# Performance work log

Hardware: AMD Instinct MI355X
Metric: run time of the kernel (lower is better)

## Reference

```python
import jax, jax.numpy as jnp
import numpy as np

B, N, E = 4, 2048, 16384
D, DM, NH, DH, FE = 10, 256, 8, 32, 9
K, KHOP, SIGMA = 30, 3, 1.5
_HOP_W = np.exp(-(np.arange(1, KHOP + 1) ** 2) / (2.0 * SIGMA ** 2))
_HOP_Z = float(_HOP_W.sum())


def _ln(x, g, b):
    mu = x.mean(-1, keepdims=True)
    var = ((x - mu) ** 2).mean(-1, keepdims=True)
    return g * (x - mu) * jax.lax.rsqrt(var + 1e-5) + b


def setup_inputs() -> dict:
    key = jax.random.key(0)
    ks = jax.random.split(key, 40)
    s = 0.02
    inp = {
        'bus_type': jax.random.randint(ks[0], (B, N), 0, 4, dtype=jnp.int32),
        'edge_index': jax.random.randint(ks[1], (B, 2, E), 0, N, dtype=jnp.int32),
        'G': 0.05 * jax.random.normal(ks[2], (B, N, N), jnp.float32),
        'Bm': 0.05 * jax.random.normal(ks[3], (B, N, N), jnp.float32),
        'P_set': jax.random.normal(ks[4], (B, N), jnp.float32),
        'Q_set': jax.random.normal(ks[5], (B, N), jnp.float32),
        'V0': jnp.stack([0.9 + 0.2 * jax.random.uniform(ks[6], (B, N)),
                         0.2 * jax.random.uniform(ks[7], (B, N)) - 0.1], -1).astype(jnp.float32),
        'edge_feat': jax.random.normal(ks[8], (B, E, FE), jnp.float32),
        'Win': s * jax.random.normal(ks[9], (2 * (4 + D), DM), jnp.float32),
        'b_in': jnp.zeros((DM,), jnp.float32),
        'Wq': s * jax.random.normal(ks[10], (DM, DM), jnp.float32),
        'bq': jnp.zeros((DM,), jnp.float32),
        'Wk': s * jax.random.normal(ks[11], (DM, DM), jnp.float32),
        'bk': jnp.zeros((DM,), jnp.float32),
        'Wv': s * jax.random.normal(ks[12], (DM, DM), jnp.float32),
        'bv': jnp.zeros((DM,), jnp.float32),
        'Wo': s * jax.random.normal(ks[13], (DM, DM), jnp.float32),
        'bo': jnp.zeros((DM,), jnp.float32),
        'We': s * jax.random.normal(ks[14], (FE, NH), jnp.float32),
        'be': jnp.zeros((NH,), jnp.float32),
        'ln1_g': jnp.ones((DM,), jnp.float32),
        'ln1_b': jnp.zeros((DM,), jnp.float32),
        'ln2_g': jnp.ones((DM,), jnp.float32),
        'ln2_b': jnp.zeros((DM,), jnp.float32),
        'Wf1': s * jax.random.normal(ks[15], (DM, 4 * DM), jnp.float32),
        'bf1': jnp.zeros((4 * DM,), jnp.float32),
        'Wf2': s * jax.random.normal(ks[16], (4 * DM, DM), jnp.float32),
        'bf2': jnp.zeros((DM,), jnp.float32),
        'Wth': s * jax.random.normal(ks[17], (K, DM, 1), jnp.float32),
        'bth': jnp.zeros((K, 1), jnp.float32),
        'Wvh': s * jax.random.normal(ks[18], (K, DM, 1), jnp.float32),
        'bvh': jnp.zeros((K, 1), jnp.float32),
        'Wm': s * jax.random.normal(ks[19], (K, DM, D), jnp.float32),
        'bm': jnp.zeros((K, D), jnp.float32),
    }
    return inp


def reference(bus_type, edge_index, G, Bm, P_set, Q_set, V0, edge_feat,
              Win, b_in, Wq, bq, Wk, bk, Wv, bv, Wo, bo, We, be,
              ln1_g, ln1_b, ln2_g, ln2_b, Wf1, bf1, Wf2, bf2,
              Wth, bth, Wvh, bvh, Wm, bm):
    slack = bus_type == 1
    pv = bus_type == 2
    p_maskf = (~slack).astype(G.dtype)            # theta updates / DP mask
    q_maskf = (~(slack | pv)).astype(G.dtype)     # v updates / DQ mask

    # electrical transition matrix T = rownorm(|Y| with zero diag), khop_source='yabs', khop_norm='row'
    A = jnp.sqrt(G * G + Bm * Bm) * (1.0 - jnp.eye(N, dtype=G.dtype))
    T = A / jnp.clip(A.sum(-1, keepdims=True), 1e-12, None)

    # flattened directed edges across batch for segment ops
    src = edge_index[:, 0, :]
    dst = edge_index[:, 1, :]
    offs = (jnp.arange(B, dtype=src.dtype) * N)[:, None]
    src_f = (src + offs).reshape(-1)
    dst_f = (dst + offs).reshape(-1)
    eb_f = (edge_feat @ We + be).reshape(-1, NH)  # per-edge per-head attention bias

    def khop(X):  # Gaussian-weighted K-hop diffusion: sum_h w_h T^h X / sum_h w_h
        Hh, acc = X, jnp.zeros_like(X)
        for hop in range(KHOP):
            Hh = jnp.einsum('bij,bjf->bif', T, Hh)
            acc = acc + float(_HOP_W[hop]) * Hh
        return acc / _HOP_Z

    def attn_block(x):  # edge-sparse multi-head self-attention + FFN
        q = (x @ Wq + bq).reshape(B * N, NH, DH)
        k = (x @ Wk + bk).reshape(B * N, NH, DH)
        vv = (x @ Wv + bv).reshape(B * N, NH, DH)
        score = (q[dst_f] * k[src_f]).sum(-1) / np.sqrt(DH) + eb_f  # [B*E, NH]
        mx = jax.ops.segment_max(score, dst_f, num_segments=B * N)
        p = jnp.exp(score - mx[dst_f])
        den = jax.ops.segment_sum(p, dst_f, num_segments=B * N)
        alpha = p / den[dst_f]
        agg = jax.ops.segment_sum(alpha[:, :, None] * vv[src_f], dst_f, num_segments=B * N)
        x = _ln(x + agg.reshape(B, N, DM) @ Wo + bo, ln1_g, ln1_b)
        h = jax.nn.relu(x @ Wf1 + bf1)
        return _ln(x + h @ Wf2 + bf2, ln2_g, ln2_b)

    def step(carry, hp):
        v, th, m = carry
        Wth_k, bth_k, Wvh_k, bvh_k, Wm_k, bm_k = hp
        e = v * jnp.cos(th)
        f = v * jnp.sin(th)
        Ire = jnp.einsum('bij,bj->bi', G, e) - jnp.einsum('bij,bj->bi', Bm, f)
        Iim = jnp.einsum('bij,bj->bi', G, f) + jnp.einsum('bij,bj->bi', Bm, e)
        DP = (P_set - (e * Ire + f * Iim)) * p_maskf
        DQ = (Q_set - (f * Ire - e * Iim)) * q_maskf
        ns = jnp.concatenate([jnp.stack([v, th, DP, DQ], -1), m], -1)  # [B,N,4+D]
        x = jnp.concatenate([ns, khop(ns)], -1) @ Win + b_in
        x = attn_block(x)
        dth = (x @ Wth_k + bth_k)[..., 0]
        dv = (x @ Wvh_k + bvh_k)[..., 0]
        m_new = x @ Wm_k + bm_k
        return (v + dv * q_maskf, th + dth * p_maskf, m_new), None

    v0, th0 = V0[..., 0], V0[..., 1]
    m0 = jnp.zeros((B, N, D), dtype=V0.dtype)
    (v, th, _), _ = jax.lax.scan(step, (v0, th0, m0), (Wth, bth, Wvh, bvh, Wm, bm))
    return jnp.stack([v, th], -1)
```

## Files before the change

kernel.cpp:

```cpp
#include <hip/hip_runtime.h>
#include <math.h>

typedef _Float16 f16x8 __attribute__((ext_vector_type(8)));
typedef _Float16 f16x4 __attribute__((ext_vector_type(4)));
typedef float f32x4 __attribute__((ext_vector_type(4)));

constexpr int B_ = 4, N_ = 2048, E_ = 16384;
constexpr int D_ = 10, DM_ = 256, NH_ = 8, FE_ = 9;
constexpr int BN_ = B_ * N_;
constexpr int BE_ = B_ * E_;

#define DEVI __device__ __forceinline__

DEVI _Float16 f2h(float f) { return (_Float16)f; }


__global__ void init_state(const int* __restrict__ bus, const float* __restrict__ V0,
                           float* v, float* th, float* m, float* pm, float* qm,
                           int* counts) {
  int t = blockIdx.x * blockDim.x + threadIdx.x;
  if (t >= BN_) return;
  int bt = bus[t];
  pm[t] = (bt == 1) ? 0.f : 1.f;
  qm[t] = (bt == 1 || bt == 2) ? 0.f : 1.f;
  v[t] = V0[2 * t];
  th[t] = V0[2 * t + 1];
  for (int d = 0; d < D_; ++d) m[(size_t)t * D_ + d] = 0.f;
  counts[t] = 0;
}

__global__ __launch_bounds__(256) void build_T_cast(const float* __restrict__ G,
    const float* __restrict__ Bm, _Float16* __restrict__ Tb,
    _Float16* __restrict__ Gh, _Float16* __restrict__ Bh) {
  int row = blockIdx.x;
  int i = row & (N_ - 1);
  const float* Gr = G + (size_t)row * N_;
  const float* Br = Bm + (size_t)row * N_;
  float a[8];
  float s = 0.f;
#pragma unroll
  for (int u = 0; u < 8; ++u) {
    int j = threadIdx.x + u * 256;
    float g = Gr[j], b = Br[j];
    if (Gh) { Gh[(size_t)row * N_ + j] = f2h(g); Bh[(size_t)row * N_ + j] = f2h(b); }
    float av = sqrtf(g * g + b * b);
    if (j == i) av = 0.f;
    a[u] = av;
    s += av;
  }
  __shared__ float red[4];
  for (int off = 32; off; off >>= 1) s += __shfl_down(s, off);
  int lane = threadIdx.x & 63, wave = threadIdx.x >> 6;
  if (lane == 0) red[wave] = s;
  __syncthreads();
  float tot = red[0] + red[1] + red[2] + red[3];
  float inv = 1.f / fmaxf(tot, 1e-12f);
#pragma unroll
  for (int u = 0; u < 8; ++u) {
    int j = threadIdx.x + u * 256;
    Tb[(size_t)row * N_ + j] = f2h(a[u] * inv);
  }
}

__global__ __launch_bounds__(256) void transpose16(const _Float16* __restrict__ in,
                                                   _Float16* __restrict__ out) {
  __shared__ float tile[64][65];
  int b = blockIdx.z;
  const _Float16* A = in + (size_t)b * N_ * N_;
  _Float16* O = out + (size_t)b * N_ * N_;
  int r0 = blockIdx.y * 64, c0 = blockIdx.x * 64;
  int tc = threadIdx.x & 63, tg = threadIdx.x >> 6;
#pragma unroll
  for (int i = 0; i < 16; ++i) {
    int r = tg * 16 + i;
    tile[r][tc] = (float)A[(size_t)(r0 + r) * N_ + c0 + tc];
  }
  __syncthreads();
#pragma unroll
  for (int i = 0; i < 16; ++i) {
    int r = tg * 16 + i;
    O[(size_t)(c0 + r) * N_ + r0 + tc] = f2h(tile[tc][r]);
  }
}

__global__ __launch_bounds__(256) void gemm_bat(const _Float16* __restrict__ A,
    const _Float16* __restrict__ Bt, _Float16* __restrict__ Cout,
    const _Float16* __restrict__ M1, const _Float16* __restrict__ M2,
    float w1, float w2, float w3) {
  int b = blockIdx.z;
  const _Float16* Ab = A + (size_t)b * N_ * N_;
  const _Float16* Bb = Bt + (size_t)b * N_ * N_;
  int wave = threadIdx.x >> 6, lane = threadIdx.x & 63;
  int wy = wave >> 1, wx = wave & 1;
  int m0 = blockIdx.x * 64 + wy * 32;
  int n0 = blockIdx.y * 64 + wx * 32;
  int lm = lane & 15, lq = lane >> 4;
  f32x4 acc[2][2] = {};
  const _Float16* A0 = Ab + (size_t)(m0 + lm) * N_ + lq * 8;
  const _Float16* A1 = A0 + (size_t)16 * N_;
  const _Float16* B0 = Bb + (size_t)(n0 + lm) * N_ + lq * 8;
  const _Float16* B1 = B0 + (size_t)16 * N_;
  for (int k = 0; k < N_; k += 32) {
    f16x8 a0 = *(const f16x8*)(A0 + k);
    f16x8 a1 = *(const f16x8*)(A1 + k);
    f16x8 b0 = *(const f16x8*)(B0 + k);
    f16x8 b1 = *(const f16x8*)(B1 + k);
    acc[0][0] = __builtin_amdgcn_mfma_f32_16x16x32_f16(a0, b0, acc[0][0], 0, 0, 0);
    acc[0][1] = __builtin_amdgcn_mfma_f32_16x16x32_f16(a0, b1, acc[0][1], 0, 0, 0);
    acc[1][0] = __builtin_amdgcn_mfma_f32_16x16x32_f16(a1, b0, acc[1][0], 0, 0, 0);
    acc[1][1] = __builtin_amdgcn_mfma_f32_16x16x32_f16(a1, b1, acc[1][1], 0, 0, 0);
  }
  _Float16* Cb = Cout + (size_t)b * N_ * N_;
#pragma unroll
  for (int tm = 0; tm < 2; ++tm)
#pragma unroll
    for (int tn = 0; tn < 2; ++tn) {
      int col = n0 + tn * 16 + lm;
#pragma unroll
      for (int r = 0; r < 4; ++r) {
        int row = m0 + tm * 16 + lq * 4 + r;
        size_t o = (size_t)b * N_ * N_ + (size_t)row * N_ + col;
        float val = acc[tm][tn][r];
        if (M1) val = w3 * val + w1 * (float)M1[o] + w2 * (float)M2[o];
        Cb[(size_t)row * N_ + col] = f2h(val);
      }
    }
}

__global__ void edge_prep(const int* __restrict__ ei, const float* __restrict__ efeat,
    const float* __restrict__ We, const float* __restrict__ be,
    float* __restrict__ eb, int* __restrict__ srcf, int* __restrict__ dstf,
    int* __restrict__ counts) {
  int t = blockIdx.x * blockDim.x + threadIdx.x;
  if (t >= BE_) return;
  int b = t / E_, e = t - b * E_;
  int src = ei[(size_t)b * 2 * E_ + e];
  int dst = ei[(size_t)b * 2 * E_ + E_ + e];
  srcf[t] = src + b * N_;
  int df = dst + b * N_;
  dstf[t] = df;
  atomicAdd(&counts[df], 1);
  float fv[FE_];
#pragma unroll
  for (int f = 0; f < FE_; ++f) fv[f] = efeat[(size_t)t * FE_ + f];
#pragma unroll
  for (int h = 0; h < NH_; ++h) {
    float s = be[h];
#pragma unroll
    for (int f = 0; f < FE_; ++f) s += fv[f] * We[f * NH_ + h];
    eb[(size_t)t * NH_ + h] = s;
  }
}

__global__ void scan_kernel(const int* __restrict__ counts, int* __restrict__ offs,
                            int* __restrict__ cursor) {
  __shared__ int part[256];
  int t = threadIdx.x;
  int base = t * 32;
  int loc[32];
  int s = 0;
#pragma unroll
  for (int i = 0; i < 32; ++i) { loc[i] = counts[base + i]; s += loc[i]; }
  part[t] = s;
  __syncthreads();
  for (int off = 1; off < 256; off <<= 1) {
    int vv = (t >= off) ? part[t - off] : 0;
    __syncthreads();
    part[t] += vv;
    __syncthreads();
  }
  int run = part[t] - s;
#pragma unroll
  for (int i = 0; i < 32; ++i) {
    offs[base + i] = run;
    cursor[base + i] = run;
    run += loc[i];
  }
  if (t == 255) offs[BN_] = run;
}

__global__ void scatter_kernel(const int* __restrict__ dstf, int* cursor,
                               int* __restrict__ perm) {
  int t = blockIdx.x * blockDim.x + threadIdx.x;
  if (t >= BE_) return;
  int d = dstf[t];
  int pos = atomicAdd(&cursor[d], 1);
  perm[pos] = t;
}

__global__ void edge_reorder(const int* __restrict__ perm, const int* __restrict__ srcf,
                             const float* __restrict__ eb, int* __restrict__ sp,
                             float* __restrict__ ebp) {
  int j = blockIdx.x * 256 + threadIdx.x;
  if (j >= BE_) return;
  int e = perm[j];
  sp[j] = srcf[e];
#pragma unroll
  for (int h = 0; h < NH_; ++h) ebp[(size_t)j * 8 + h] = eb[(size_t)e * 8 + h];
}

__global__ void prep_weights(const float* Wq, const float* bq, const float* Wk,
    const float* bk, const float* Wv, const float* bvv, const float* Wo,
    const float* Wf1, const float* Wf2, const float* Wth, const float* bth,
    const float* Wvh, const float* bvh, const float* Wm, const float* bm,
    const float* Win,
    _Float16* Wqkvt, float* bqkv, _Float16* Wot,
    _Float16* Wf1t, _Float16* Wf2t, float* Wheads, float* bheads,
    _Float16* Wint) {
  int i = blockIdx.x * blockDim.x + threadIdx.x;
  if (i < 768 * 256) {
    int n = i >> 8, kk = i & 255;
    float val = n < 256 ? Wq[kk * 256 + n]
              : n < 512 ? Wk[kk * 256 + (n - 256)] : Wv[kk * 256 + (n - 512)];
    Wqkvt[n * 256 + kk] = f2h(val);
    return;
  }
  i -= 768 * 256;
  if (i < 256 * 256) {
    int n = i >> 8, kk = i & 255;
    Wot[n * 256 + kk] = f2h(Wo[kk * 256 + n]);
    return;
  }
  i -= 256 * 256;
  if (i < 1024 * 256) {
    int n = i >> 8, kk = i & 255;
    Wf1t[n * 256 + kk] = f2h(Wf1[kk * 1024 + n]);
    return;
  }
  i -= 1024 * 256;
  if (i < 256 * 1024) {
    int n = i >> 10, kk = i & 1023;
    Wf2t[n * 1024 + kk] = f2h(Wf2[kk * 256 + n]);
    return;
  }
  i -= 256 * 1024;
  if (i < 30 * 3072) {
    int k = i / 3072, j = i - k * 3072;
    int row = j / 12, o = j - row * 12;
    float val = o == 0 ? Wth[k * 256 + row]
              : o == 1 ? Wvh[k * 256 + row] : Wm[k * 2560 + row * 10 + (o - 2)];
    Wheads[k * 3072 + j] = val;
    return;
  }
  i -= 30 * 3072;
  if (i < 360) {
    int k = i / 12, o = i - k * 12;
    bheads[i] = o == 0 ? bth[k] : o == 1 ? bvh[k] : bm[k * 10 + (o - 2)];
    return;
  }
  i -= 360;
  if (i < 768) {
    bqkv[i] = i < 256 ? bq[i] : i < 512 ? bk[i - 256] : bvv[i - 512];
    return;
  }
  i -= 768;
  if (i < 256 * 32) {
    int n = i >> 5, kk = i & 31;
    Wint[n * 32 + kk] = (kk < 28) ? f2h(Win[kk * 256 + n]) : (_Float16)0.f;
  }
}


DEVI void ns_epilogue(int b, int row, float sre, float sim, int lane,
                      const float2* sef, const float* v, const float* th,
                      const float* P, const float* Q, const float* pm,
                      const float* qm, const float* m, _Float16* nsT) {
  for (int off = 1; off < 64; off <<= 1) {
    sre += __shfl_xor(sre, off);
    sim += __shfl_xor(sim, off);
  }
  if (lane < 16) {
    int node = b * N_ + row;
    float val;
    if (lane == 0) val = v[node];
    else if (lane == 1) val = th[node];
    else if (lane == 2) {
      float2 ef = sef[row];
      val = (P[node] - (ef.x * sre + ef.y * sim)) * pm[node];
    } else if (lane == 3) {
      float2 ef = sef[row];
      val = (Q[node] - (ef.y * sre - ef.x * sim)) * qm[node];
    } else if (lane < 14) val = m[(size_t)node * 10 + (lane - 4)];
    else val = 0.f;
    nsT[(size_t)b * 16 * N_ + (size_t)lane * N_ + row] = f2h(val);
  }
}

__global__ __launch_bounds__(256) void matvec_ns_f16(const _Float16* __restrict__ Gh,
    const _Float16* __restrict__ Bh, const float* __restrict__ v,
    const float* __restrict__ th, const float* __restrict__ P,
    const float* __restrict__ Q, const float* __restrict__ pm,
    const float* __restrict__ qm, const float* __restrict__ m,
    _Float16* __restrict__ nsT) {
  int b = blockIdx.y;
  __shared__ float2 sef[N_];
  for (int i = threadIdx.x; i < N_; i += 256) {
    float vv = v[b * N_ + i], tt = th[b * N_ + i];
    float sn, cs;
    __sincosf(tt, &sn, &cs);
    sef[i] = make_float2(vv * cs, vv * sn);
  }
  __syncthreads();
  int wave = threadIdx.x >> 6, lane = threadIdx.x & 63;
  for (int rr = 0; rr < 4; ++rr) {
    int row = blockIdx.x * 16 + wave * 4 + rr;
    const _Float16* Gr = Gh + ((size_t)b * N_ + row) * N_;
    const _Float16* Br = Bh + ((size_t)b * N_ + row) * N_;
    float sre = 0.f, sim = 0.f;
#pragma unroll
    for (int jj = 0; jj < 4; ++jj) {
      int j = lane * 8 + jj * 512;
      f16x8 g8 = *(const f16x8*)(Gr + j);
      f16x8 b8 = *(const f16x8*)(Br + j);
#pragma unroll
      for (int u = 0; u < 8; ++u) {
        float g = (float)g8[u], bb = (float)b8[u];
        float2 ef = sef[j + u];
        sre += g * ef.x - bb * ef.y;
        sim += g * ef.y + bb * ef.x;
      }
    }
    ns_epilogue(b, row, sre, sim, lane, sef, v, th, P, Q, pm, qm, m, nsT);
  }
}

__global__ __launch_bounds__(256) void matvec_ns_f32(const float* __restrict__ G,
    const float* __restrict__ Bm, const float* __restrict__ v,
    const float* __restrict__ th, const float* __restrict__ P,
    const float* __restrict__ Q, const float* __restrict__ pm,
    const float* __restrict__ qm, const float* __restrict__ m,
    _Float16* __restrict__ nsT) {
  int b = blockIdx.y;
  __shared__ float2 sef[N_];
  for (int i = threadIdx.x; i < N_; i += 256) {
    float vv = v[b * N_ + i], tt = th[b * N_ + i];
    float sn, cs;
    __sincosf(tt, &sn, &cs);
    sef[i] = make_float2(vv * cs, vv * sn);
  }
  __syncthreads();
  int wave = threadIdx.x >> 6, lane = threadIdx.x & 63;
  for (int rr = 0; rr < 4; ++rr) {
    int row = blockIdx.x * 16 + wave * 4 + rr;
    const float* Gr = G + ((size_t)b * N_ + row) * N_;
    const float* Br = Bm + ((size_t)b * N_ + row) * N_;
    float sre = 0.f, sim = 0.f;
#pragma unroll
    for (int jj = 0; jj < 8; ++jj) {
      int j = lane * 4 + jj * 256;
      float4 g4 = *(const float4*)(Gr + j);
      float4 b4 = *(const float4*)(Br + j);
      float2 e0 = sef[j], e1 = sef[j + 1], e2 = sef[j + 2], e3 = sef[j + 3];
      sre += g4.x * e0.x - b4.x * e0.y + g4.y * e1.x - b4.y * e1.y
           + g4.z * e2.x - b4.z * e2.y + g4.w * e3.x - b4.w * e3.y;
      sim += g4.x * e0.y + b4.x * e0.x + g4.y * e1.y + b4.y * e1.x
           + g4.z * e2.y + b4.z * e2.x + g4.w * e3.y + b4.w * e3.x;
    }
    ns_epilogue(b, row, sre, sim, lane, sef, v, th, P, Q, pm, qm, m, nsT);
  }
}

DEVI float khop_tile(const _Float16* __restrict__ Tm, const _Float16* __restrict__ Hin,
                     int b, int m0, int wave, int lm, int lq, int tid,
                     float (*red)[16][17]) {
  f32x4 acc = {0.f, 0.f, 0.f, 0.f};
  const _Float16* Trow = Tm + ((size_t)b * N_ + m0 + lm) * N_ + wave * 512 + lq * 8;
  const _Float16* Hrow = Hin + ((size_t)b * 16 + lm) * N_ + wave * 512 + lq * 8;
#pragma unroll 4
  for (int k = 0; k < 512; k += 32) {
    f16x8 a = *(const f16x8*)(Trow + k);
    f16x8 hb = *(const f16x8*)(Hrow + k);
    acc = __builtin_amdgcn_mfma_f32_16x16x32_f16(a, hb, acc, 0, 0, 0);
  }
#pragma unroll
  for (int r = 0; r < 4; ++r) red[wave][lq * 4 + r][lm] = acc[r];
  __syncthreads();
  int c = tid >> 4, rr = tid & 15;
  float s = red[0][rr][c] + red[1][rr][c] + red[2][rr][c] + red[3][rr][c];
  __syncthreads();
  return s;
}

__global__ __launch_bounds__(256) void khop_mix_input(
    const _Float16* __restrict__ Tmix, const _Float16* __restrict__ nsT,
    const _Float16* __restrict__ Wint, const float* __restrict__ bin,
    float* __restrict__ x0, _Float16* __restrict__ xh) {
  int b = blockIdx.y, m0 = blockIdx.x * 16;
  int tid = threadIdx.x;
  int wave = tid >> 6, lane = tid & 63;
  int lm = lane & 15, lq = lane >> 4;
  __shared__ float red[4][16][17];
  __shared__ _Float16 in28s[16][32];
  float s = khop_tile(Tmix, nsT, b, m0, wave, lm, lq, tid, red);
  int oc = tid >> 4, orr = tid & 15;
  size_t oidx = ((size_t)b * 16 + oc) * N_ + m0 + orr;
  if (oc < 14) {
    in28s[orr][oc] = nsT[oidx];
    in28s[orr][14 + oc] = f2h(s);
  } else if (oc == 14) {
    in28s[orr][28] = (_Float16)0.f;
    in28s[orr][29] = (_Float16)0.f;
  } else {
    in28s[orr][30] = (_Float16)0.f;
    in28s[orr][31] = (_Float16)0.f;
  }
  __syncthreads();
  f16x8 afrag = *(const f16x8*)(&in28s[lm][lq * 8]);
#pragma unroll
  for (int nt = 0; nt < 4; ++nt) {
    int n0 = wave * 64 + nt * 16;
    f16x8 bfrag = *(const f16x8*)(Wint + (size_t)(n0 + lm) * 32 + lq * 8);
    f32x4 c4 = {0.f, 0.f, 0.f, 0.f};
    c4 = __builtin_amdgcn_mfma_f32_16x16x32_f16(afrag, bfrag, c4, 0, 0, 0);
    float bv = bin[n0 + lm];
#pragma unroll
    for (int rg = 0; rg < 4; ++rg) {
      int rw = lq * 4 + rg;
      float val = c4[rg] + bv;
      size_t o = ((size_t)(b * N_ + m0 + rw)) * 256 + n0 + lm;
      x0[o] = val;
      xh[o] = f2h(val);
    }
  }
}

__global__ __launch_bounds__(256) void khop_kernel(const _Float16* __restrict__ Tb,
    const _Float16* __restrict__ HinT, _Float16* __restrict__ HoutT,
    float* __restrict__ accT, float w, int first) {
  int b = blockIdx.y, m0 = blockIdx.x * 16;
  int tid = threadIdx.x;
  int wave = tid >> 6, lane = tid & 63;
  int lm = lane & 15, lq = lane >> 4;
  __shared__ float red[4][16][17];
  float s = khop_tile(Tb, HinT, b, m0, wave, lm, lq, tid, red);
  int c = tid >> 4, r = tid & 15;
  size_t o = ((size_t)b * 16 + c) * N_ + m0 + r;
  if (HoutT) HoutT[o] = f2h(s);
  if (first) accT[o] = w * s; else accT[o] += w * s;
}

__global__ __launch_bounds__(256) void khop3_input(const _Float16* __restrict__ Tb,
    const _Float16* __restrict__ HinT, const _Float16* __restrict__ nsT,
    const float* __restrict__ accT, const _Float16* __restrict__ Wint,
    const float* __restrict__ bin, float hw2,
    float* __restrict__ x0, _Float16* __restrict__ xh) {
  int b = blockIdx.y, m0 = blockIdx.x * 16;
  int tid = threadIdx.x;
  int wave = tid >> 6, lane = tid & 63;
  int lm = lane & 15, lq = lane >> 4;
  __shared__ float red[4][16][17];
  __shared__ _Float16 in28s[16][32];
  float s = khop_tile(Tb, HinT, b, m0, wave, lm, lq, tid, red);
  int oc = tid >> 4, orr = tid & 15;
  size_t oidx = ((size_t)b * 16 + oc) * N_ + m0 + orr;
  if (oc < 14) {
    float atot = accT[oidx] + hw2 * s;
    in28s[orr][oc] = nsT[oidx];
    in28s[orr][14 + oc] = f2h(atot);
  } else if (oc == 14) {
    in28s[orr][28] = (_Float16)0.f;
    in28s[orr][29] = (_Float16)0.f;
  } else {
    in28s[orr][30] = (_Float16)0.f;
    in28s[orr][31] = (_Float16)0.f;
  }
  __syncthreads();
  f16x8 afrag = *(const f16x8*)(&in28s[lm][lq * 8]);
#pragma unroll
  for (int nt = 0; nt < 4; ++nt) {
    int n0 = wave * 64 + nt * 16;
    f16x8 bfrag = *(const f16x8*)(Wint + (size_t)(n0 + lm) * 32 + lq * 8);
    f32x4 c4 = {0.f, 0.f, 0.f, 0.f};
    c4 = __builtin_amdgcn_mfma_f32_16x16x32_f16(afrag, bfrag, c4, 0, 0, 0);
    float bv = bin[n0 + lm];
#pragma unroll
    for (int rg = 0; rg < 4; ++rg) {
      int rw = lq * 4 + rg;
      float val = c4[rg] + bv;
      size_t o = ((size_t)(b * N_ + m0 + rw)) * 256 + n0 + lm;
      x0[o] = val;
      xh[o] = f2h(val);
    }
  }
}

__global__ __launch_bounds__(256) void gemm_kernel(const _Float16* __restrict__ A,
    const _Float16* __restrict__ Wt, const float* __restrict__ bias,
    float* __restrict__ Cf, _Float16* __restrict__ Ch,
    int N, int K, int relu) {
  int wave = threadIdx.x >> 6, lane = threadIdx.x & 63;
  int wy = wave >> 1, wx = wave & 1;
  int m0 = blockIdx.x * 64 + wy * 32;
  int n0 = blockIdx.y * 64 + wx * 32;
  int lm = lane & 15, lq = lane >> 4;
  f32x4 acc[2][2] = {};
  const _Float16* A0 = A + (size_t)(m0 + lm) * K + lq * 8;
  const _Float16* A1 = A0 + (size_t)16 * K;
  const _Float16* B0 = Wt + (size_t)(n0 + lm) * K + lq * 8;
  const _Float16* B1 = B0 + (size_t)16 * K;
  for (int k = 0; k < K; k += 32) {
    f16x8 a0 = *(const f16x8*)(A0 + k);
    f16x8 a1 = *(const f16x8*)(A1 + k);
    f16x8 b0 = *(const f16x8*)(B0 + k);
    f16x8 b1 = *(const f16x8*)(B1 + k);
    acc[0][0] = __builtin_amdgcn_mfma_f32_16x16x32_f16(a0, b0, acc[0][0], 0, 0, 0);
    acc[0][1] = __builtin_amdgcn_mfma_f32_16x16x32_f16(a0, b1, acc[0][1], 0, 0, 0);
    acc[1][0] = __builtin_amdgcn_mfma_f32_16x16x32_f16(a1, b0, acc[1][0], 0, 0, 0);
    acc[1][1] = __builtin_amdgcn_mfma_f32_16x16x32_f16(a1, b1, acc[1][1], 0, 0, 0);
  }
#pragma unroll
  for (int tm = 0; tm < 2; ++tm)
#pragma unroll
    for (int tn = 0; tn < 2; ++tn) {
      int col = n0 + tn * 16 + lm;
      float bvv = bias ? bias[col] : 0.f;
#pragma unroll
      for (int r = 0; r < 4; ++r) {
        int row = m0 + tm * 16 + lq * 4 + r;
        float val = acc[tm][tn][r] + bvv;
        if (relu) val = fmaxf(val, 0.f);
        size_t o = (size_t)row * N + col;
        if (Cf) Cf[o] = val;
        if (Ch) Ch[o] = f2h(val);
      }
    }
}

__global__ __launch_bounds__(256) void attn_kernel(const _Float16* __restrict__ qkv,
    const int* __restrict__ offs, const int* __restrict__ sp,
    const float* __restrict__ ebp, _Float16* __restrict__ aggh) {
  int node = blockIdx.x * 4 + (threadIdx.x >> 6);
  int lane = threadIdx.x & 63;
  int h = lane >> 3;
  f16x4 qh = *(const f16x4*)(qkv + (size_t)node * 768 + lane * 4);
  float4 q4 = {(float)qh[0], (float)qh[1], (float)qh[2], (float)qh[3]};
  int beg = offs[node], end = offs[node + 1];
  float mx = -3.0e38f, den = 0.f;
  float4 acc = {0.f, 0.f, 0.f, 0.f};
  f16x4 kh_n = {}, vh_n = {};
  float eb_n = 0.f;
  if (beg < end) {
    int s = sp[beg];
    const _Float16* base = qkv + (size_t)s * 768 + lane * 4;
    kh_n = *(const f16x4*)(base + 256);
    vh_n = *(const f16x4*)(base + 512);
    eb_n = ebp[(size_t)beg * 8 + h];
  }
  for (int j = beg; j < end; ++j) {
    f16x4 kh = kh_n, vh = vh_n;
    float ebv = eb_n;
    if (j + 1 < end) {
      int s2 = sp[j + 1];
      const _Float16* b2 = qkv + (size_t)s2 * 768 + lane * 4;
      kh_n = *(const f16x4*)(b2 + 256);
      vh_n = *(const f16x4*)(b2 + 512);
      eb_n = ebp[(size_t)(j + 1) * 8 + h];
    }
    float p = q4.x * (float)kh[0] + q4.y * (float)kh[1]
            + q4.z * (float)kh[2] + q4.w * (float)kh[3];
    p += __shfl_xor(p, 1);
    p += __shfl_xor(p, 2);
    p += __shfl_xor(p, 4);
    float score = p * 0.17677669529663687f + ebv;
    float nm = fmaxf(mx, score);
    float sc = __expf(mx - nm);
    float w = __expf(score - nm);
    den = den * sc + w;
    acc.x = acc.x * sc + w * (float)vh[0];
    acc.y = acc.y * sc + w * (float)vh[1];
    acc.z = acc.z * sc + w * (float)vh[2];
    acc.w = acc.w * sc + w * (float)vh[3];
    mx = nm;
  }
  float inv = den > 0.f ? 1.f / den : 0.f;
  f16x4 o;
  o[0] = f2h(acc.x * inv);
  o[1] = f2h(acc.y * inv);
  o[2] = f2h(acc.z * inv);
  o[3] = f2h(acc.w * inv);
  *(f16x4*)(aggh + (size_t)node * DM_ + lane * 4) = o;
}

__global__ __launch_bounds__(256) void oproj_ln1(const _Float16* __restrict__ A,
    const _Float16* __restrict__ Wt, const float* __restrict__ bias,
    const float* __restrict__ res, const float* __restrict__ g,
    const float* __restrict__ bb, float* __restrict__ yF,
    _Float16* __restrict__ yH) {
  int m0 = blockIdx.x * 16;
  int wave = threadIdx.x >> 6, lane = threadIdx.x & 63;
  int lm = lane & 15, lq = lane >> 4;
  int n0 = wave * 64;
  f32x4 acc[4] = {};
  const _Float16* Ap = A + (size_t)(m0 + lm) * 256 + lq * 8;
  const _Float16* Bp = Wt + (size_t)(n0 + lm) * 256 + lq * 8;
  for (int k = 0; k < 256; k += 32) {
    f16x8 a0 = *(const f16x8*)(Ap + k);
#pragma unroll
    for (int nt = 0; nt < 4; ++nt) {
      f16x8 bf = *(const f16x8*)(Bp + nt * 16 * 256 + k);
      acc[nt] = __builtin_amdgcn_mfma_f32_16x16x32_f16(a0, bf, acc[nt], 0, 0, 0);
    }
  }
  float val[4][4];
  float rsum[4] = {}, rsq[4] = {};
#pragma unroll
  for (int nt = 0; nt < 4; ++nt) {
    int col = n0 + nt * 16 + lm;
    float bv = bias[col];
#pragma unroll
    for (int rg = 0; rg < 4; ++rg) {
      int row = m0 + lq * 4 + rg;
      float x = acc[nt][rg] + bv + res[(size_t)row * 256 + col];
      val[nt][rg] = x;
      rsum[rg] += x;
      rsq[rg] += x * x;
    }
  }
#pragma unroll
  for (int rg = 0; rg < 4; ++rg)
    for (int off = 1; off < 16; off <<= 1) {
      rsum[rg] += __shfl_xor(rsum[rg], off);
      rsq[rg] += __shfl_xor(rsq[rg], off);
    }
  __shared__ float redS[16][4], redQ[16][4];
  if (lm == 0) {
#pragma unroll
    for (int rg = 0; rg < 4; ++rg) {
      int r = lq * 4 + rg;
      redS[r][wave] = rsum[rg];
      redQ[r][wave] = rsq[rg];
    }
  }
  __syncthreads();
#pragma unroll
  for (int rg = 0; rg < 4; ++rg) {
    int r = lq * 4 + rg;
    float tS = redS[r][0] + redS[r][1] + redS[r][2] + redS[r][3];
    float tQ = redQ[r][0] + redQ[r][1] + redQ[r][2] + redQ[r][3];
    float mu = tS * (1.f / 256.f);
    float var = tQ * (1.f / 256.f) - mu * mu;
    float rs = rsqrtf(var + 1e-5f);
    int row = m0 + r;
#pragma unroll
    for (int nt = 0; nt < 4; ++nt) {
      int col = n0 + nt * 16 + lm;
      float y = g[col] * (val[nt][rg] - mu) * rs + bb[col];
      size_t o = (size_t)row * 256 + col;
      yF[o] = y;
      yH[o] = f2h(y);
    }
  }
}

__global__ __launch_bounds__(512) void ffn_fused(const _Float16* __restrict__ A,
    const _Float16* __restrict__ Wf1t, const float* __restrict__ bf1,
    const _Float16* __restrict__ Wf2t, const float* __restrict__ bf2,
    const float* __restrict__ res, const float* __restrict__ g,
    const float* __restrict__ bb, const float* __restrict__ Wh,
    const float* __restrict__ bh, const float* __restrict__ pm,
    const float* __restrict__ qm, float* __restrict__ v,
    float* __restrict__ th, float* __restrict__ m) {
  constexpr int HP = 1032;
  int m0 = blockIdx.x * 32;
  int tid = threadIdx.x;
  int wave = tid >> 6, lane = tid & 63;
  int lm = lane & 15, lq = lane >> 4;
  __shared__ _Float16 hs[32][HP];
  __shared__ float xs[32][261];
  __shared__ float whs[3072];
  __shared__ float part[32][193];
  __shared__ float redS[32][8], redQ[32][8];
  for (int i = tid; i < 3072; i += 512) whs[i] = Wh[i];
  {
    int n0 = wave * 128;
    f32x4 acc1[2][8] = {};
    const _Float16* Ap = A + (size_t)(m0 + lm) * 256 + lq * 8;
    const _Float16* Bp = Wf1t + (size_t)(n0 + lm) * 256 + lq * 8;
    for (int k = 0; k < 256; k += 32) {
      f16x8 a0 = *(const f16x8*)(Ap + k);
      f16x8 a1 = *(const f16x8*)(Ap + 16 * 256 + k);
#pragma unroll
      for (int nt = 0; nt < 8; ++nt) {
        f16x8 bf = *(const f16x8*)(Bp + nt * 16 * 256 + k);
        acc1[0][nt] = __builtin_amdgcn_mfma_f32_16x16x32_f16(a0, bf, acc1[0][nt], 0, 0, 0);
        acc1[1][nt] = __builtin_amdgcn_mfma_f32_16x16x32_f16(a1, bf, acc1[1][nt], 0, 0, 0);
      }
    }
#pragma unroll
    for (int mt = 0; mt < 2; ++mt)
#pragma unroll
      for (int nt = 0; nt < 8; ++nt) {
        int col = n0 + nt * 16 + lm;
        float bv = bf1[col];
#pragma unroll
        for (int rg = 0; rg < 4; ++rg) {
          int rloc = mt * 16 + lq * 4 + rg;
          hs[rloc][col] = f2h(fmaxf(acc1[mt][nt][rg] + bv, 0.f));
        }
      }
  }
  __syncthreads();
  float val[2][2][4];
  float rsum[2][4] = {}, rsq[2][4] = {};
  {
    int n0 = wave * 32;
    f32x4 acc2[2][2] = {};
    const _Float16* Bp = Wf2t + (size_t)(n0 + lm) * 1024 + lq * 8;
    for (int k = 0; k < 1024; k += 32) {
      f16x8 a0 = *(const f16x8*)(&hs[lm][k + lq * 8]);
      f16x8 a1 = *(const f16x8*)(&hs[16 + lm][k + lq * 8]);
      f16x8 b0 = *(const f16x8*)(Bp + k);
      f16x8 b1 = *(const f16x8*)(Bp + 16 * 1024 + k);
      acc2[0][0] = __builtin_amdgcn_mfma_f32_16x16x32_f16(a0, b0, acc2[0][0], 0, 0, 0);
      acc2[0][1] = __builtin_amdgcn_mfma_f32_16x16x32_f16(a0, b1, acc2[0][1], 0, 0, 0);
      acc2[1][0] = __builtin_amdgcn_mfma_f32_16x16x32_f16(a1, b0, acc2[1][0], 0, 0, 0);
      acc2[1][1] = __builtin_amdgcn_mfma_f32_16x16x32_f16(a1, b1, acc2[1][1], 0, 0, 0);
    }
#pragma unroll
    for (int mt = 0; mt < 2; ++mt)
#pragma unroll
      for (int nt = 0; nt < 2; ++nt) {
        int col = n0 + nt * 16 + lm;
        float bv = bf2[col];
#pragma unroll
        for (int rg = 0; rg < 4; ++rg) {
          int row = m0 + mt * 16 + lq * 4 + rg;
          float x = acc2[mt][nt][rg] + bv + res[(size_t)row * 256 + col];
          val[mt][nt][rg] = x;
          rsum[mt][rg] += x;
          rsq[mt][rg] += x * x;
        }
      }
  }
#pragma unroll
  for (int mt = 0; mt < 2; ++mt)
#pragma unroll
    for (int rg = 0; rg < 4; ++rg)
      for (int off = 1; off < 16; off <<= 1) {
        rsum[mt][rg] += __shfl_xor(rsum[mt][rg], off);
        rsq[mt][rg] += __shfl_xor(rsq[mt][rg], off);
      }
  if (lm == 0) {
#pragma unroll
    for (int mt = 0; mt < 2; ++mt)
#pragma unroll
      for (int rg = 0; rg < 4; ++rg) {
        int r = mt * 16 + lq * 4 + rg;
        redS[r][wave] = rsum[mt][rg];
        redQ[r][wave] = rsq[mt][rg];
      }
  }
  __syncthreads();
#pragma unroll
  for (int mt = 0; mt < 2; ++mt)
#pragma unroll
    for (int rg = 0; rg < 4; ++rg) {
      int r = mt * 16 + lq * 4 + rg;
      float tS = 0.f, tQ = 0.f;
#pragma unroll
      for (int w = 0; w < 8; ++w) { tS += redS[r][w]; tQ += redQ[r][w]; }
      float mu = tS * (1.f / 256.f);
      float var = tQ * (1.f / 256.f) - mu * mu;
      float rs = rsqrtf(var + 1e-5f);
#pragma unroll
      for (int nt = 0; nt < 2; ++nt) {
        int col = wave * 32 + nt * 16 + lm;
        xs[r][col] = g[col] * (val[mt][nt][rg] - mu) * rs + bb[col];
      }
    }
  __syncthreads();
  {
    int rw = tid & 31, grp = tid >> 5;
    float pa[12] = {};
    for (int c = 0; c < 16; ++c) {
      int col = grp * 16 + c;
      float xv = xs[rw][col];
#pragma unroll
      for (int o = 0; o < 12; ++o) pa[o] += xv * whs[col * 12 + o];
    }
#pragma unroll
    for (int o = 0; o < 12; ++o) part[rw][grp * 12 + o] = pa[o];
  }
  __syncthreads();
  if (tid < 32) {
    int node = m0 + tid;
    float tot[12];
#pragma unroll
    for (int o = 0; o < 12; ++o) {
      float s = bh[o];
#pragma unroll
      for (int grp = 0; grp < 16; ++grp) s += part[tid][grp * 12 + o];
      tot[o] = s;
    }
    th[node] += tot[0] * pm[node];
    v[node] += tot[1] * qm[node];
#pragma unroll
    for (int d = 0; d < 10; ++d) m[(size_t)node * 10 + d] = tot[2 + d];
  }
}

__global__ void out_kernel(const float* __restrict__ v, const float* __restrict__ th,
                           float* __restrict__ out) {
  int t = blockIdx.x * blockDim.x + threadIdx.x;
  if (t >= BN_) return;
  out[2 * t] = v[t];
  out[2 * t + 1] = th[t];
}


extern "C" void kernel_launch(void* const* d_in, const int* in_sizes, int n_in,
                              void* d_out, int out_size, void* d_ws, size_t ws_size,
                              hipStream_t stream) {
  const int* bus = (const int*)d_in[0];
  const int* ei = (const int*)d_in[1];
  const float* G = (const float*)d_in[2];
  const float* Bm = (const float*)d_in[3];
  const float* P = (const float*)d_in[4];
  const float* Q = (const float*)d_in[5];
  const float* V0 = (const float*)d_in[6];
  const float* efeat = (const float*)d_in[7];
  const float* Win = (const float*)d_in[8];
  const float* bin = (const float*)d_in[9];
  const float* Wq = (const float*)d_in[10];
  const float* bq = (const float*)d_in[11];
  const float* Wk = (const float*)d_in[12];
  const float* bk = (const float*)d_in[13];
  const float* Wv = (const float*)d_in[14];
  const float* bv = (const float*)d_in[15];
  const float* Wo = (const float*)d_in[16];
  const float* bo = (const float*)d_in[17];
  const float* We = (const float*)d_in[18];
  const float* be = (const float*)d_in[19];
  const float* g1 = (const float*)d_in[20];
  const float* b1 = (const float*)d_in[21];
  const float* g2 = (const float*)d_in[22];
  const float* b2 = (const float*)d_in[23];
  const float* Wf1 = (const float*)d_in[24];
  const float* bf1 = (const float*)d_in[25];
  const float* Wf2 = (const float*)d_in[26];
  const float* bf2 = (const float*)d_in[27];
  const float* Wth = (const float*)d_in[28];
  const float* bth = (const float*)d_in[29];
  const float* Wvh = (const float*)d_in[30];
  const float* bvh = (const float*)d_in[31];
  const float* Wm = (const float*)d_in[32];
  const float* bm = (const float*)d_in[33];
  float* out = (float*)d_out;

  char* p = (char*)d_ws;
  auto alloc = [&](size_t bytes) -> void* {
    void* r = (void*)p;
    p += (bytes + 255) & ~(size_t)255;
    return r;
  };
  _Float16* Tb = (_Float16*)alloc((size_t)BN_ * N_ * 2);
  _Float16* nsT = (_Float16*)alloc((size_t)B_ * 16 * N_ * 2);
  _Float16* H1 = (_Float16*)alloc((size_t)B_ * 16 * N_ * 2);
  _Float16* H2 = (_Float16*)alloc((size_t)B_ * 16 * N_ * 2);
  float* accT = (float*)alloc((size_t)B_ * 16 * N_ * 4);
  _Float16* qkvh = (_Float16*)alloc((size_t)BN_ * 768 * 2);
  float* x0 = (float*)alloc((size_t)BN_ * 256 * 4);
  float* x1 = (float*)alloc((size_t)BN_ * 256 * 4);
  _Float16* xhA = (_Float16*)alloc((size_t)BN_ * 256 * 2);
  _Float16* xhB = (_Float16*)alloc((size_t)BN_ * 256 * 2);
  float* eb = (float*)alloc((size_t)BE_ * 8 * 4);
  float* ebp = (float*)alloc((size_t)BE_ * 8 * 4);
  int* srcf = (int*)alloc((size_t)BE_ * 4);
  int* dstf = (int*)alloc((size_t)BE_ * 4);
  int* sp = (int*)alloc((size_t)BE_ * 4);
  int* counts = (int*)alloc((size_t)BN_ * 4);
  int* offs = (int*)alloc((size_t)(BN_ + 1) * 4);
  int* cursor = (int*)alloc((size_t)BN_ * 4);
  int* perm = (int*)alloc((size_t)BE_ * 4);
  _Float16* Wqkvt = (_Float16*)alloc(768 * 256 * 2);
  _Float16* Wot = (_Float16*)alloc(256 * 256 * 2);
  _Float16* Wf1t = (_Float16*)alloc(1024 * 256 * 2);
  _Float16* Wf2t = (_Float16*)alloc(256 * 1024 * 2);
  _Float16* Wint = (_Float16*)alloc(256 * 32 * 2);
  float* Wheads = (float*)alloc(30 * 3072 * 4);
  float* bheads = (float*)alloc(30 * 12 * 4);
  float* bqkv = (float*)alloc(768 * 4);
  float* v = (float*)alloc((size_t)BN_ * 4);
  float* th = (float*)alloc((size_t)BN_ * 4);
  float* pm = (float*)alloc((size_t)BN_ * 4);
  float* qm = (float*)alloc((size_t)BN_ * 4);
  float* m = (float*)alloc((size_t)BN_ * 10 * 4);

  size_t nn2 = (size_t)B_ * N_ * N_ * 2;
  size_t used = (size_t)(p - (char*)d_ws);
  bool tmix_ok = (used + 3 * (nn2 + 256) <= ws_size);
  _Float16 *Tt = nullptr, *T2 = nullptr, *Tmix = nullptr;
  if (tmix_ok) {
    Tt = (_Float16*)alloc(nn2);
    T2 = (_Float16*)alloc(nn2);
    Tmix = (_Float16*)alloc(nn2);
  }
  used = (size_t)(p - (char*)d_ws);
  bool f16gb = (used + 2 * (nn2 + 256) <= ws_size);
  _Float16 *Gh = nullptr, *Bh = nullptr;
  if (f16gb) {
    Gh = (_Float16*)alloc(nn2);
    Bh = (_Float16*)alloc(nn2);
  }

  double hwd[3], z = 0.0;
  for (int i = 0; i < 3; ++i) {
    hwd[i] = exp(-((double)(i + 1) * (i + 1)) / (2.0 * 1.5 * 1.5));
    z += hwd[i];
  }
  float hw0 = (float)(hwd[0] / z), hw1 = (float)(hwd[1] / z), hw2 = (float)(hwd[2] / z);

  init_state<<<32, 256, 0, stream>>>(bus, V0, v, th, m, pm, qm, counts);
  build_T_cast<<<8192, 256, 0, stream>>>(G, Bm, Tb, Gh, Bh);
  if (tmix_ok) {
    transpose16<<<dim3(32, 32, 4), 256, 0, stream>>>(Tb, Tt);
    gemm_bat<<<dim3(32, 32, 4), 256, 0, stream>>>(Tb, Tt, T2,
        (const _Float16*)nullptr, (const _Float16*)nullptr, 0.f, 0.f, 0.f);
    gemm_bat<<<dim3(32, 32, 4), 256, 0, stream>>>(T2, Tt, Tmix, Tb, T2,
                                                  hw0, hw1, hw2);
  }
  edge_prep<<<BE_ / 256, 256, 0, stream>>>(ei, efeat, We, be, eb, srcf, dstf, counts);
  scan_kernel<<<1, 256, 0, stream>>>(counts, offs, cursor);
  scatter_kernel<<<BE_ / 256, 256, 0, stream>>>(dstf, cursor, perm);
  edge_reorder<<<BE_ / 256, 256, 0, stream>>>(perm, srcf, eb, sp, ebp);
  prep_weights<<<(887912 + 255) / 256, 256, 0, stream>>>(
      Wq, bq, Wk, bk, Wv, bv, Wo, Wf1, Wf2, Wth, bth, Wvh, bvh, Wm, bm, Win,
      Wqkvt, bqkv, Wot, Wf1t, Wf2t, Wheads, bheads, Wint);

  for (int k = 0; k < 30; ++k) {
    if (f16gb)
      matvec_ns_f16<<<dim3(128, 4), 256, 0, stream>>>(Gh, Bh, v, th, P, Q, pm, qm,
                                                      m, nsT);
    else
      matvec_ns_f32<<<dim3(128, 4), 256, 0, stream>>>(G, Bm, v, th, P, Q, pm, qm,
                                                      m, nsT);
    if (tmix_ok) {
      khop_mix_input<<<dim3(128, 4), 256, 0, stream>>>(Tmix, nsT, Wint, bin,
                                                       x0, xhA);
    } else {
      khop_kernel<<<dim3(128, 4), 256, 0, stream>>>(Tb, nsT, H1, accT, hw0, 1);
      khop_kernel<<<dim3(128, 4), 256, 0, stream>>>(Tb, H1, H2, accT, hw1, 0);
      khop3_input<<<dim3(128, 4), 256, 0, stream>>>(Tb, H2, nsT, accT, Wint, bin,
                                                    hw2, x0, xhA);
    }
    gemm_kernel<<<dim3(128, 12), 256, 0, stream>>>(xhA, Wqkvt, bqkv, nullptr, qkvh,
                                                   768, 256, 0);
    attn_kernel<<<2048, 256, 0, stream>>>(qkvh, offs, sp, ebp, xhB);
    oproj_ln1<<<512, 256, 0, stream>>>(xhB, Wot, bo, x0, g1, b1, x1, xhA);
    ffn_fused<<<256, 512, 0, stream>>>(xhA, Wf1t, bf1, Wf2t, bf2, x1, g2, b2,
                                       Wheads + k * 3072, bheads + k * 12,
                                       pm, qm, v, th, m);
  }
  out_kernel<<<32, 256, 0, stream>>>(v, th, out);
}
```

Before: 4.791 ms.

## Enlarge batched GEMM tiles to 128x128 and overlay FFN shared buffers

The batched T·T GEMM used to precompute the k-hop mixing matrix now gives each wave a 64x64 output tile, 4x4 MFMA accumulators, instead of 32x32. The launch grid shrinks to match. This quarters the number of blocks and raises register-level reuse of each loaded A/B fragment, cutting redundant global loads. In the fused FFN kernel, the f16 hidden buffer and the later LayerNorm/head buffers now share one union in LDS, and the head-weight load moves after the second GEMM. This lowers shared-memory footprint, which could allow more blocks per CU. The costs are higher register pressure in the GEMM and fewer blocks to fill the GPU.

Result: faster. 4.618 ms (-3.6%).

```diff
diff --git a/kernel.cpp b/kernel.cpp
--- a/kernel.cpp
+++ b/kernel.cpp
@@ -92,35 +92,38 @@
   const _Float16* Bb = Bt + (size_t)b * N_ * N_;
   int wave = threadIdx.x >> 6, lane = threadIdx.x & 63;
   int wy = wave >> 1, wx = wave & 1;
-  int m0 = blockIdx.x * 64 + wy * 32;
-  int n0 = blockIdx.y * 64 + wx * 32;
+  int m0 = blockIdx.x * 128 + wy * 64;
+  int n0 = blockIdx.y * 128 + wx * 64;
   int lm = lane & 15, lq = lane >> 4;
-  f32x4 acc[2][2] = {};
-  const _Float16* A0 = Ab + (size_t)(m0 + lm) * N_ + lq * 8;
-  const _Float16* A1 = A0 + (size_t)16 * N_;
-  const _Float16* B0 = Bb + (size_t)(n0 + lm) * N_ + lq * 8;
-  const _Float16* B1 = B0 + (size_t)16 * N_;
+  f32x4 acc[4][4] = {};
+  const _Float16* Ap0 = Ab + (size_t)(m0 + lm) * N_ + lq * 8;
+  const _Float16* Bp0 = Bb + (size_t)(n0 + lm) * N_ + lq * 8;
+#pragma unroll 2
   for (int k = 0; k < N_; k += 32) {
-    f16x8 a0 = *(const f16x8*)(A0 + k);
-    f16x8 a1 = *(const f16x8*)(A1 + k);
-    f16x8 b0 = *(const f16x8*)(B0 + k);
-    f16x8 b1 = *(const f16x8*)(B1 + k);
-    acc[0][0] = __builtin_amdgcn_mfma_f32_16x16x32_f16(a0, b0, acc[0][0], 0, 0, 0);
-    acc[0][1] = __builtin_amdgcn_mfma_f32_16x16x32_f16(a0, b1, acc[0][1], 0, 0, 0);
-    acc[1][0] = __builtin_amdgcn_mfma_f32_16x16x32_f16(a1, b0, acc[1][0], 0, 0, 0);
-    acc[1][1] = __builtin_amdgcn_mfma_f32_16x16x32_f16(a1, b1, acc[1][1], 0, 0, 0);
+    f16x8 af[4], bf[4];
+#pragma unroll
+    for (int i = 0; i < 4; ++i) {
+      af[i] = *(const f16x8*)(Ap0 + (size_t)i * 16 * N_ + k);
+      bf[i] = *(const f16x8*)(Bp0 + (size_t)i * 16 * N_ + k);
+    }
+#pragma unroll
+    for (int mi = 0; mi < 4; ++mi)
+#pragma unroll
+      for (int ni = 0; ni < 4; ++ni)
+        acc[mi][ni] = __builtin_amdgcn_mfma_f32_16x16x32_f16(af[mi], bf[ni],
+                                                             acc[mi][ni], 0, 0, 0);
   }
   _Float16* Cb = Cout + (size_t)b * N_ * N_;
 #pragma unroll
-  for (int tm = 0; tm < 2; ++tm)
-#pragma unroll
-    for (int tn = 0; tn < 2; ++tn) {
-      int col = n0 + tn * 16 + lm;
+  for (int mi = 0; mi < 4; ++mi)
+#pragma unroll
+    for (int ni = 0; ni < 4; ++ni) {
+      int col = n0 + ni * 16 + lm;
 #pragma unroll
       for (int r = 0; r < 4; ++r) {
-        int row = m0 + tm * 16 + lq * 4 + r;
+        int row = m0 + mi * 16 + lq * 4 + r;
         size_t o = (size_t)b * N_ * N_ + (size_t)row * N_ + col;
-        float val = acc[tm][tn][r];
+        float val = acc[mi][ni][r];
         if (M1) val = w3 * val + w1 * (float)M1[o] + w2 * (float)M2[o];
         Cb[(size_t)row * N_ + col] = f2h(val);
       }
@@ -652,6 +655,16 @@
   }
 }
 
+struct FfnS2 {
+  float xs[32][261];
+  float whs[3072];
+  float part[32][193];
+};
+union FfnU {
+  _Float16 hs[32][1040];
+  FfnS2 s2;
+};
+
 __global__ __launch_bounds__(512) void ffn_fused(const _Float16* __restrict__ A,
     const _Float16* __restrict__ Wf1t, const float* __restrict__ bf1,
     const _Float16* __restrict__ Wf2t, const float* __restrict__ bf2,
@@ -660,17 +673,13 @@
     const float* __restrict__ bh, const float* __restrict__ pm,
     const float* __restrict__ qm, float* __restrict__ v,
     float* __restrict__ th, float* __restrict__ m) {
-  constexpr int HP = 1032;
+  constexpr int HP = 1040;
   int m0 = blockIdx.x * 32;
   int tid = threadIdx.x;
   int wave = tid >> 6, lane = tid & 63;
   int lm = lane & 15, lq = lane >> 4;
-  __shared__ _Float16 hs[32][HP];
-  __shared__ float xs[32][261];
-  __shared__ float whs[3072];
-  __shared__ float part[32][193];
+  __shared__ FfnU u;
   __shared__ float redS[32][8], redQ[32][8];
-  for (int i = tid; i < 3072; i += 512) whs[i] = Wh[i];
   {
     int n0 = wave * 128;
     f32x4 acc1[2][8] = {};
@@ -695,7 +704,7 @@
 #pragma unroll
         for (int rg = 0; rg < 4; ++rg) {
           int rloc = mt * 16 + lq * 4 + rg;
-          hs[rloc][col] = f2h(fmaxf(acc1[mt][nt][rg] + bv, 0.f));
+          u.hs[rloc][col] = f2h(fmaxf(acc1[mt][nt][rg] + bv, 0.f));
         }
       }
   }
@@ -707,8 +716,8 @@
     f32x4 acc2[2][2] = {};
     const _Float16* Bp = Wf2t + (size_t)(n0 + lm) * 1024 + lq * 8;
     for (int k = 0; k < 1024; k += 32) {
-      f16x8 a0 = *(const f16x8*)(&hs[lm][k + lq * 8]);
-      f16x8 a1 = *(const f16x8*)(&hs[16 + lm][k + lq * 8]);
+      f16x8 a0 = *(const f16x8*)(&u.hs[lm][k + lq * 8]);
+      f16x8 a1 = *(const f16x8*)(&u.hs[16 + lm][k + lq * 8]);
       f16x8 b0 = *(const f16x8*)(Bp + k);
       f16x8 b1 = *(const f16x8*)(Bp + 16 * 1024 + k);
       acc2[0][0] = __builtin_amdgcn_mfma_f32_16x16x32_f16(a0, b0, acc2[0][0], 0, 0, 0);
@@ -751,6 +760,7 @@
       }
   }
   __syncthreads();
+  for (int i = tid; i < 3072; i += 512) u.s2.whs[i] = Wh[i];
 #pragma unroll
   for (int mt = 0; mt < 2; ++mt)
 #pragma unroll
@@ -765,7 +775,7 @@
 #pragma unroll
       for (int nt = 0; nt < 2; ++nt) {
         int col = wave * 32 + nt * 16 + lm;
-        xs[r][col] = g[col] * (val[mt][nt][rg] - mu) * rs + bb[col];
+        u.s2.xs[r][col] = g[col] * (val[mt][nt][rg] - mu) * rs + bb[col];
       }
     }
   __syncthreads();
@@ -774,12 +784,12 @@
     float pa[12] = {};
     for (int c = 0; c < 16; ++c) {
       int col = grp * 16 + c;
-      float xv = xs[rw][col];
-#pragma unroll
-      for (int o = 0; o < 12; ++o) pa[o] += xv * whs[col * 12 + o];
-    }
-#pragma unroll
-    for (int o = 0; o < 12; ++o) part[rw][grp * 12 + o] = pa[o];
+      float xv = u.s2.xs[rw][col];
+#pragma unroll
+      for (int o = 0; o < 12; ++o) pa[o] += xv * u.s2.whs[col * 12 + o];
+    }
+#pragma unroll
+    for (int o = 0; o < 12; ++o) u.s2.part[rw][grp * 12 + o] = pa[o];
   }
   __syncthreads();
   if (tid < 32) {
@@ -789,7 +799,7 @@
     for (int o = 0; o < 12; ++o) {
       float s = bh[o];
 #pragma unroll
-      for (int grp = 0; grp < 16; ++grp) s += part[tid][grp * 12 + o];
+      for (int grp = 0; grp < 16; ++grp) s += u.s2.part[tid][grp * 12 + o];
       tot[o] = s;
     }
     th[node] += tot[0] * pm[node];
@@ -914,9 +924,9 @@
   build_T_cast<<<8192, 256, 0, stream>>>(G, Bm, Tb, Gh, Bh);
   if (tmix_ok) {
     transpose16<<<dim3(32, 32, 4), 256, 0, stream>>>(Tb, Tt);
-    gemm_bat<<<dim3(32, 32, 4), 256, 0, stream>>>(Tb, Tt, T2,
+    gemm_bat<<<dim3(16, 16, 4), 256, 0, stream>>>(Tb, Tt, T2,
         (const _Float16*)nullptr, (const _Float16*)nullptr, 0.f, 0.f, 0.f);
-    gemm_bat<<<dim3(32, 32, 4), 256, 0, stream>>>(T2, Tt, Tmix, Tb, T2,
+    gemm_bat<<<dim3(16, 16, 4), 256, 0, stream>>>(T2, Tt, Tmix, Tb, T2,
                                                   hw0, hw1, hw2);
   }
   edge_prep<<<BE_ / 256, 256, 0, stream>>>(ei, efeat, We, be, eb, srcf, dstf, counts);
```
